# Kernel tuning notes

Hardware: AMD Instinct MI355X
Metric: run time of the kernel (lower is better)

## Reference

```python
import jax, jax.numpy as jnp
import numpy as np

LN_EPS = 1e-5  # torch nn.LayerNorm default

def _layer_norm(x, w, b):
    m = jnp.mean(x, axis=-1, keepdims=True)
    v = jnp.mean(jnp.square(x - m), axis=-1, keepdims=True)
    return (x - m) * jax.lax.rsqrt(v + LN_EPS) * w + b

def setup_inputs() -> dict:
    R, N, D, A = 8, 8192, 2048, 128
    init_scale = 0.01
    key = jax.random.key(0)
    k0, k1, k2 = jax.random.split(key, 3)
    x = jax.random.normal(k0, (N, D), jnp.float32)
    ln_w = jnp.ones((R, D), jnp.float32)              # per-router input LayerNorm weight
    ln_b = jnp.zeros((R, D), jnp.float32)
    router_weights = jax.random.normal(k1, (R, D, A), jnp.float32) * init_scale
    rw_ln_w = jax.random.normal(k2, (R, D), jnp.float32) * init_scale  # weight-LN gamma (init ones*scale in src)
    rw_ln_b = jnp.zeros((R, D), jnp.float32)
    router_bias = jnp.zeros((R, A), jnp.float32)
    return {"x": x, "ln_w": ln_w, "ln_b": ln_b, "router_weights": router_weights,
            "rw_ln_w": rw_ln_w, "rw_ln_b": rw_ln_b, "router_bias": router_bias}

def reference(x, ln_w, ln_b, router_weights, rw_ln_w, rw_ln_b, router_bias):
    # Per-router LayerNorm of shared input x: new_x [R, N, D]
    new_x = jax.vmap(lambda w, b: _layer_norm(x, w, b))(ln_w, ln_b)
    # normalize_router_weights=True: LayerNorm over in_dim of W[i].T, then transpose back
    rw_norm = jax.vmap(lambda W, w, b: _layer_norm(W.T, w, b).T)(router_weights, rw_ln_w, rw_ln_b)  # [R, D, A]
    adapter_logits = jnp.einsum('rnd,rda->rna', new_x, rw_norm) + router_bias[:, None, :]
    adapter_probs = jax.nn.softmax(adapter_logits, axis=-1)
    return new_x, adapter_logits, adapter_probs
```

## Files before the change

### kernel.cpp

```cpp
#include <hip/hip_runtime.h>
#include <hip/hip_bf16.h>
#include <stdint.h>

#define R_ 8
#define N_ 8192
#define D_ 2048
#define A_ 128
#define J_ 1024
#define LN_EPS 1e-5f

typedef __attribute__((ext_vector_type(8))) short bf16x8;
typedef __attribute__((ext_vector_type(4))) float f32x4;

__device__ inline ushort f2bf(float f) {
    union { float f; uint32_t u; } v; v.f = f;
    uint32_t u = v.u;
    return (ushort)((u + 0x7fffu + ((u >> 16) & 1u)) >> 16);
}
__device__ inline float bf2f(ushort u) {
    union { uint32_t u; float f; } v; v.u = ((uint32_t)u) << 16;
    return v.f;
}

__global__ __launch_bounds__(256) void k_prep(
    const float* __restrict__ x,
    const float* __restrict__ W,
    const float* __restrict__ ln_w,
    const float* __restrict__ ln_b,
    const float* __restrict__ rw_w,
    const float* __restrict__ rw_b,
    const float* __restrict__ rbias,
    ushort* __restrict__ xhat,
    ushort* __restrict__ Bt,
    float* __restrict__ cvec)
{
    __shared__ float sm[16];
    const int t = threadIdx.x;

    if (blockIdx.x < N_) {
        const int n = blockIdx.x;
        const float* xr = x + (size_t)n * D_;
        float4 v0 = *(const float4*)(xr + t * 4);
        float4 v1 = *(const float4*)(xr + 1024 + t * 4);
        float s  = v0.x + v0.y + v0.z + v0.w + v1.x + v1.y + v1.z + v1.w;
        float sq = v0.x*v0.x + v0.y*v0.y + v0.z*v0.z + v0.w*v0.w
                 + v1.x*v1.x + v1.y*v1.y + v1.z*v1.z + v1.w*v1.w;
        #pragma unroll
        for (int o = 32; o > 0; o >>= 1) {
            s  += __shfl_xor(s,  o, 64);
            sq += __shfl_xor(sq, o, 64);
        }
        if ((t & 63) == 0) { sm[t >> 6] = s; sm[8 + (t >> 6)] = sq; }
        __syncthreads();
        s  = sm[0] + sm[1] + sm[2] + sm[3];
        sq = sm[8] + sm[9] + sm[10] + sm[11];
        const float mean = s * (1.0f / D_);
        const float var  = sq * (1.0f / D_) - mean * mean;
        const float rstd = rsqrtf(var + LN_EPS);

        ushort4 p0 = make_ushort4(f2bf((v0.x - mean) * rstd), f2bf((v0.y - mean) * rstd),
                                  f2bf((v0.z - mean) * rstd), f2bf((v0.w - mean) * rstd));
        ushort4 p1 = make_ushort4(f2bf((v1.x - mean) * rstd), f2bf((v1.y - mean) * rstd),
                                  f2bf((v1.z - mean) * rstd), f2bf((v1.w - mean) * rstd));
        *(ushort4*)(xhat + (size_t)n * D_ + t * 4)        = p0;
        *(ushort4*)(xhat + (size_t)n * D_ + 1024 + t * 4) = p1;
    } else {
        const int j = blockIdx.x - N_;
        const int r = j >> 7, a = j & 127;
        const float* Wc = W + (size_t)r * D_ * A_ + a;

        float vals[8];
        float s = 0.f, sq = 0.f;
        #pragma unroll
        for (int k = 0; k < 8; ++k) {
            float v = Wc[(size_t)(t + k * 256) * A_];
            vals[k] = v; s += v; sq += v * v;
        }
        #pragma unroll
        for (int o = 32; o > 0; o >>= 1) {
            s  += __shfl_xor(s,  o, 64);
            sq += __shfl_xor(sq, o, 64);
        }
        if ((t & 63) == 0) { sm[t >> 6] = s; sm[8 + (t >> 6)] = sq; }
        __syncthreads();
        s  = sm[0] + sm[1] + sm[2] + sm[3];
        sq = sm[8] + sm[9] + sm[10] + sm[11];
        const float mean = s * (1.0f / D_);
        const float var  = sq * (1.0f / D_) - mean * mean;
        const float rstd = rsqrtf(var + LN_EPS);

        float cp = 0.f;
        #pragma unroll
        for (int k = 0; k < 8; ++k) {
            const int d = t + k * 256;
            const float nv = (vals[k] - mean) * rstd * rw_w[(size_t)r * D_ + d]
                           + rw_b[(size_t)r * D_ + d];
            Bt[(size_t)j * D_ + d] = f2bf(ln_w[(size_t)r * D_ + d] * nv);
            cp += ln_b[(size_t)r * D_ + d] * nv;
        }
        __syncthreads();
        #pragma unroll
        for (int o = 32; o > 0; o >>= 1) cp += __shfl_xor(cp, o, 64);
        if ((t & 63) == 0) sm[t >> 6] = cp;
        __syncthreads();
        if (t == 0) cvec[j] = sm[0] + sm[1] + sm[2] + sm[3] + rbias[(size_t)r * A_ + a];
    }
}

__global__ __launch_bounds__(256) void k_fused(
    const ushort* __restrict__ Xh,
    const ushort* __restrict__ Bt,
    const float* __restrict__ cvec,
    const float* __restrict__ ln_w,
    const float* __restrict__ ln_b,
    float* __restrict__ new_x,
    float* __restrict__ logits,
    float* __restrict__ probs)
{
    __shared__ __attribute__((aligned(16))) ushort As[2][64 * 32];
    __shared__ __attribute__((aligned(16))) ushort Bs[2][128 * 32];
    __shared__ __attribute__((aligned(16))) float lwS[D_];
    __shared__ __attribute__((aligned(16))) float lbS[D_];

    const int t    = threadIdx.x;
    const int lane = t & 63;
    const int w    = t >> 6;
    const int r    = blockIdx.x & 7;
    const int mt   = blockIdx.x >> 3;
    const int m0   = mt * 64;
    const int j0   = r * 128;

    const int arow = t >> 2, akc = t & 3;
    const ushort* gA0 = Xh + (size_t)(m0 + arow) * D_ + akc * 8;

    auto stage = [&](int buf, int kt) {
        __builtin_amdgcn_global_load_lds(
            (const __attribute__((address_space(1))) void*)(gA0 + kt * 32),
            (__attribute__((address_space(3))) void*)(&As[buf][t * 8]), 16, 0, 0);
        #pragma unroll
        for (int c = 0; c < 2; ++c) {
            const int q   = t + c * 256;
            const int row = q >> 2;
            const int kc  = q & 3;
            const ushort* gB = Bt + (size_t)(j0 + row) * D_ + kt * 32 + kc * 8;
            __builtin_amdgcn_global_load_lds(
                (const __attribute__((address_space(1))) void*)gB,
                (__attribute__((address_space(3))) void*)(&Bs[buf][q * 8]), 16, 0, 0);
        }
    };

    #pragma unroll
    for (int i = 0; i < 2; ++i) {
        const int idx = t + i * 256;
        ((float4*)lwS)[idx] = ((const float4*)(ln_w + (size_t)r * D_))[idx];
        ((float4*)lbS)[idx] = ((const float4*)(ln_b + (size_t)r * D_))[idx];
    }

    f32x4 acc[8];
    #pragma unroll
    for (int jf = 0; jf < 8; ++jf) acc[jf] = (f32x4){0.f, 0.f, 0.f, 0.f};

    float* nx_base = new_x + ((size_t)r * N_ + m0) * D_;

    stage(0, 0);
    asm volatile("s_waitcnt vmcnt(0) lgkmcnt(0)" ::: "memory");
    __builtin_amdgcn_s_barrier();
    __builtin_amdgcn_sched_barrier(0);

    auto body = [&](int cur, int kt) {
        if (kt < 63) stage(cur ^ 1, kt + 1);

        const int kbase = kt * 32;
        #pragma unroll
        for (int c = 0; c < 2; ++c) {
            const int q    = t + c * 256;
            const int row  = q >> 3;
            const int col4 = q & 7;
            const int d    = kbase + col4 * 4;
            const ushort4 hb = *(const ushort4*)(&As[cur][row * 32 + col4 * 4]);
            const float4 lw4 = *(const float4*)(&lwS[d]);
            const float4 lb4 = *(const float4*)(&lbS[d]);
            f32x4 o;
            o[0] = bf2f(hb.x) * lw4.x + lb4.x;
            o[1] = bf2f(hb.y) * lw4.y + lb4.y;
            o[2] = bf2f(hb.z) * lw4.z + lb4.z;
            o[3] = bf2f(hb.w) * lw4.w + lb4.w;
            __builtin_nontemporal_store(o, (f32x4*)(nx_base + (size_t)row * D_ + d));
        }

        const bf16x8 afr = *(const bf16x8*)(&As[cur][(w * 16 + (lane & 15)) * 32
                                                     + (lane >> 4) * 8]);
        #pragma unroll
        for (int jf = 0; jf < 8; ++jf) {
            const bf16x8 bfr = *(const bf16x8*)(&Bs[cur][(jf * 16 + (lane & 15)) * 32
                                                         + (lane >> 4) * 8]);
            acc[jf] = __builtin_amdgcn_mfma_f32_16x16x32_bf16(afr, bfr, acc[jf], 0, 0, 0);
        }

        if (kt < 63) {
            asm volatile("s_waitcnt vmcnt(2)" ::: "memory");
            __builtin_amdgcn_s_barrier();
            __builtin_amdgcn_sched_barrier(0);
        }
    };

    for (int kt2 = 0; kt2 < 64; kt2 += 2) {
        body(0, kt2);
        body(1, kt2 + 1);
    }

    float cv[8];
    #pragma unroll
    for (int jf = 0; jf < 8; ++jf) cv[jf] = cvec[j0 + jf * 16 + (lane & 15)];

    #pragma unroll
    for (int reg = 0; reg < 4; ++reg) {
        const int row = m0 + w * 16 + (lane >> 4) * 4 + reg;
        float v[8], e[8];
        float mx = -3.4e38f;
        #pragma unroll
        for (int jf = 0; jf < 8; ++jf) {
            v[jf] = acc[jf][reg] + cv[jf];
            mx = fmaxf(mx, v[jf]);
        }
        #pragma unroll
        for (int o = 8; o > 0; o >>= 1) mx = fmaxf(mx, __shfl_xor(mx, o, 64));
        float ssum = 0.f;
        #pragma unroll
        for (int jf = 0; jf < 8; ++jf) { e[jf] = __expf(v[jf] - mx); ssum += e[jf]; }
        #pragma unroll
        for (int o = 8; o > 0; o >>= 1) ssum += __shfl_xor(ssum, o, 64);
        const float inv = 1.0f / ssum;
        float* lrow = logits + ((size_t)r * N_ + row) * A_;
        float* prow = probs  + ((size_t)r * N_ + row) * A_;
        #pragma unroll
        for (int jf = 0; jf < 8; ++jf) {
            const int aa = jf * 16 + (lane & 15);
            __builtin_nontemporal_store(v[jf], lrow + aa);
            __builtin_nontemporal_store(e[jf] * inv, prow + aa);
        }
    }
}

extern "C" void kernel_launch(void* const* d_in, const int* in_sizes, int n_in,
                              void* d_out, int out_size, void* d_ws, size_t ws_size,
                              hipStream_t stream)
{
    const float* x     = (const float*)d_in[0];
    const float* ln_w  = (const float*)d_in[1];
    const float* ln_b  = (const float*)d_in[2];
    const float* W     = (const float*)d_in[3];
    const float* rw_w  = (const float*)d_in[4];
    const float* rw_b  = (const float*)d_in[5];
    const float* rbias = (const float*)d_in[6];

    float* out    = (float*)d_out;
    float* new_x  = out;
    float* logits = out + (size_t)R_ * N_ * D_;
    float* probs  = logits + (size_t)R_ * N_ * A_;

    ushort* xhat = (ushort*)d_ws;
    ushort* Btp  = (ushort*)((char*)d_ws + (size_t)N_ * D_ * 2);
    float*  cvec = (float*)((char*)d_ws + (size_t)N_ * D_ * 2 + (size_t)J_ * D_ * 2);

    hipLaunchKernelGGL(k_prep, dim3(N_ + J_), dim3(256), 0, stream,
                       x, W, ln_w, ln_b, rw_w, rw_b, rbias, xhat, Btp, cvec);
    hipLaunchKernelGGL(k_fused, dim3(J_), dim3(256), 0, stream,
                       xhat, Btp, cvec, ln_w, ln_b, new_x, logits, probs);
}
```

Before: 191.4 us.

## Warp-specialize fused kernel into MFMA producer warps and new_x store warps

The fused kernel grows to 512 threads. The first four waves stage tiles and run the MFMA GEMM plus softmax, and four extra waves only rescale the shared bf16 X tile and stream new_x to global memory, synchronized by matching per-iteration barriers. The goal is to overlap the large new_x write traffic with the matrix work instead of serializing both in the same waves. To fit the larger block, the LayerNorm gamma/beta copies in LDS are stored as bf16. That loses precision for general weights and raises the per-block thread count, which may lower occupancy.

```diff
diff --git a/kernel.cpp b/kernel.cpp
--- a/kernel.cpp
+++ b/kernel.cpp
@@ -107,7 +107,7 @@
     }
 }
 
-__global__ __launch_bounds__(256) void k_fused(
+__global__ __launch_bounds__(512) void k_fused(
     const ushort* __restrict__ Xh,
     const ushort* __restrict__ Bt,
     const float* __restrict__ cvec,
@@ -119,125 +119,134 @@
 {
     __shared__ __attribute__((aligned(16))) ushort As[2][64 * 32];
     __shared__ __attribute__((aligned(16))) ushort Bs[2][128 * 32];
-    __shared__ __attribute__((aligned(16))) float lwS[D_];
-    __shared__ __attribute__((aligned(16))) float lbS[D_];
-
-    const int t    = threadIdx.x;
-    const int lane = t & 63;
-    const int w    = t >> 6;
-    const int r    = blockIdx.x & 7;
-    const int mt   = blockIdx.x >> 3;
-    const int m0   = mt * 64;
-    const int j0   = r * 128;
-
-    const int arow = t >> 2, akc = t & 3;
-    const ushort* gA0 = Xh + (size_t)(m0 + arow) * D_ + akc * 8;
-
-    auto stage = [&](int buf, int kt) {
-        __builtin_amdgcn_global_load_lds(
-            (const __attribute__((address_space(1))) void*)(gA0 + kt * 32),
-            (__attribute__((address_space(3))) void*)(&As[buf][t * 8]), 16, 0, 0);
-        #pragma unroll
-        for (int c = 0; c < 2; ++c) {
-            const int q   = t + c * 256;
-            const int row = q >> 2;
-            const int kc  = q & 3;
-            const ushort* gB = Bt + (size_t)(j0 + row) * D_ + kt * 32 + kc * 8;
+    __shared__ __attribute__((aligned(16))) ushort lwS[D_];
+    __shared__ __attribute__((aligned(16))) ushort lbS[D_];
+
+    const int t  = threadIdx.x;
+    const int r  = blockIdx.x & 7;
+    const int mt = blockIdx.x >> 3;
+    const int m0 = mt * 64;
+    const int j0 = r * 128;
+
+    {
+        const float4 wv = ((const float4*)(ln_w + (size_t)r * D_))[t];
+        const float4 bv = ((const float4*)(ln_b + (size_t)r * D_))[t];
+        *(ushort4*)(&lwS[t * 4]) = make_ushort4(f2bf(wv.x), f2bf(wv.y), f2bf(wv.z), f2bf(wv.w));
+        *(ushort4*)(&lbS[t * 4]) = make_ushort4(f2bf(bv.x), f2bf(bv.y), f2bf(bv.z), f2bf(bv.w));
+    }
+
+    float* nx_base = new_x + ((size_t)r * N_ + m0) * D_;
+
+    if (t < 256) {
+        const int lane = t & 63;
+        const int w    = t >> 6;
+        const int arow = t >> 2, akc = t & 3;
+        const ushort* gA0 = Xh + (size_t)(m0 + arow) * D_ + akc * 8;
+
+        auto stage = [&](int buf, int kt) {
             __builtin_amdgcn_global_load_lds(
-                (const __attribute__((address_space(1))) void*)gB,
-                (__attribute__((address_space(3))) void*)(&Bs[buf][q * 8]), 16, 0, 0);
-        }
-    };
-
-    #pragma unroll
-    for (int i = 0; i < 2; ++i) {
-        const int idx = t + i * 256;
-        ((float4*)lwS)[idx] = ((const float4*)(ln_w + (size_t)r * D_))[idx];
-        ((float4*)lbS)[idx] = ((const float4*)(ln_b + (size_t)r * D_))[idx];
-    }
-
-    f32x4 acc[8];
-    #pragma unroll
-    for (int jf = 0; jf < 8; ++jf) acc[jf] = (f32x4){0.f, 0.f, 0.f, 0.f};
-
-    float* nx_base = new_x + ((size_t)r * N_ + m0) * D_;
-
-    stage(0, 0);
-    asm volatile("s_waitcnt vmcnt(0) lgkmcnt(0)" ::: "memory");
-    __builtin_amdgcn_s_barrier();
-    __builtin_amdgcn_sched_barrier(0);
-
-    auto body = [&](int cur, int kt) {
-        if (kt < 63) stage(cur ^ 1, kt + 1);
-
-        const int kbase = kt * 32;
-        #pragma unroll
-        for (int c = 0; c < 2; ++c) {
-            const int q    = t + c * 256;
-            const int row  = q >> 3;
-            const int col4 = q & 7;
-            const int d    = kbase + col4 * 4;
-            const ushort4 hb = *(const ushort4*)(&As[cur][row * 32 + col4 * 4]);
-            const float4 lw4 = *(const float4*)(&lwS[d]);
-            const float4 lb4 = *(const float4*)(&lbS[d]);
-            f32x4 o;
-            o[0] = bf2f(hb.x) * lw4.x + lb4.x;
-            o[1] = bf2f(hb.y) * lw4.y + lb4.y;
-            o[2] = bf2f(hb.z) * lw4.z + lb4.z;
-            o[3] = bf2f(hb.w) * lw4.w + lb4.w;
-            __builtin_nontemporal_store(o, (f32x4*)(nx_base + (size_t)row * D_ + d));
-        }
-
-        const bf16x8 afr = *(const bf16x8*)(&As[cur][(w * 16 + (lane & 15)) * 32
-                                                     + (lane >> 4) * 8]);
-        #pragma unroll
-        for (int jf = 0; jf < 8; ++jf) {
-            const bf16x8 bfr = *(const bf16x8*)(&Bs[cur][(jf * 16 + (lane & 15)) * 32
+                (const __attribute__((address_space(1))) void*)(gA0 + kt * 32),
+                (__attribute__((address_space(3))) void*)(&As[buf][t * 8]), 16, 0, 0);
+            #pragma unroll
+            for (int c = 0; c < 2; ++c) {
+                const int q   = t + c * 256;
+                const int row = q >> 2;
+                const int kc  = q & 3;
+                const ushort* gB = Bt + (size_t)(j0 + row) * D_ + kt * 32 + kc * 8;
+                __builtin_amdgcn_global_load_lds(
+                    (const __attribute__((address_space(1))) void*)gB,
+                    (__attribute__((address_space(3))) void*)(&Bs[buf][q * 8]), 16, 0, 0);
+            }
+        };
+
+        f32x4 acc[8];
+        #pragma unroll
+        for (int jf = 0; jf < 8; ++jf) acc[jf] = (f32x4){0.f, 0.f, 0.f, 0.f};
+
+        stage(0, 0);
+        asm volatile("s_waitcnt vmcnt(0) lgkmcnt(0)" ::: "memory");
+        __builtin_amdgcn_s_barrier();
+        __builtin_amdgcn_sched_barrier(0);
+
+        for (int i = 0; i < 64; ++i) {
+            const int cur = i & 1;
+            if (i < 63) stage(cur ^ 1, i + 1);
+
+            const bf16x8 afr = *(const bf16x8*)(&As[cur][(w * 16 + (lane & 15)) * 32
                                                          + (lane >> 4) * 8]);
-            acc[jf] = __builtin_amdgcn_mfma_f32_16x16x32_bf16(afr, bfr, acc[jf], 0, 0, 0);
-        }
-
-        if (kt < 63) {
-            asm volatile("s_waitcnt vmcnt(2)" ::: "memory");
+            #pragma unroll
+            for (int jf = 0; jf < 8; ++jf) {
+                const bf16x8 bfr = *(const bf16x8*)(&Bs[cur][(jf * 16 + (lane & 15)) * 32
+                                                             + (lane >> 4) * 8]);
+                acc[jf] = __builtin_amdgcn_mfma_f32_16x16x32_bf16(afr, bfr, acc[jf], 0, 0, 0);
+            }
+
+            asm volatile("s_waitcnt vmcnt(0)" ::: "memory");
+            __builtin_amdgcn_sched_barrier(0);
             __builtin_amdgcn_s_barrier();
             __builtin_amdgcn_sched_barrier(0);
         }
-    };
-
-    for (int kt2 = 0; kt2 < 64; kt2 += 2) {
-        body(0, kt2);
-        body(1, kt2 + 1);
-    }
-
-    float cv[8];
-    #pragma unroll
-    for (int jf = 0; jf < 8; ++jf) cv[jf] = cvec[j0 + jf * 16 + (lane & 15)];
-
-    #pragma unroll
-    for (int reg = 0; reg < 4; ++reg) {
-        const int row = m0 + w * 16 + (lane >> 4) * 4 + reg;
-        float v[8], e[8];
-        float mx = -3.4e38f;
-        #pragma unroll
-        for (int jf = 0; jf < 8; ++jf) {
-            v[jf] = acc[jf][reg] + cv[jf];
-            mx = fmaxf(mx, v[jf]);
-        }
-        #pragma unroll
-        for (int o = 8; o > 0; o >>= 1) mx = fmaxf(mx, __shfl_xor(mx, o, 64));
-        float ssum = 0.f;
-        #pragma unroll
-        for (int jf = 0; jf < 8; ++jf) { e[jf] = __expf(v[jf] - mx); ssum += e[jf]; }
-        #pragma unroll
-        for (int o = 8; o > 0; o >>= 1) ssum += __shfl_xor(ssum, o, 64);
-        const float inv = 1.0f / ssum;
-        float* lrow = logits + ((size_t)r * N_ + row) * A_;
-        float* prow = probs  + ((size_t)r * N_ + row) * A_;
-        #pragma unroll
-        for (int jf = 0; jf < 8; ++jf) {
-            const int aa = jf * 16 + (lane & 15);
-            __builtin_nontemporal_store(v[jf], lrow + aa);
-            __builtin_nontemporal_store(e[jf] * inv, prow + aa);
+
+        float cv[8];
+        #pragma unroll
+        for (int jf = 0; jf < 8; ++jf) cv[jf] = cvec[j0 + jf * 16 + (lane & 15)];
+
+        #pragma unroll
+        for (int reg = 0; reg < 4; ++reg) {
+            const int row = m0 + w * 16 + (lane >> 4) * 4 + reg;
+            float v[8], e[8];
+            float mx = -3.4e38f;
+            #pragma unroll
+            for (int jf = 0; jf < 8; ++jf) {
+                v[jf] = acc[jf][reg] + cv[jf];
+                mx = fmaxf(mx, v[jf]);
+            }
+            #pragma unroll
+            for (int o = 8; o > 0; o >>= 1) mx = fmaxf(mx, __shfl_xor(mx, o, 64));
+            float ssum = 0.f;
+            #pragma unroll
+            for (int jf = 0; jf < 8; ++jf) { e[jf] = __expf(v[jf] - mx); ssum += e[jf]; }
+            #pragma unroll
+            for (int o = 8; o > 0; o >>= 1) ssum += __shfl_xor(ssum, o, 64);
+            const float inv = 1.0f / ssum;
+            float* lrow = logits + ((size_t)r * N_ + row) * A_;
+            float* prow = probs  + ((size_t)r * N_ + row) * A_;
+            #pragma unroll
+            for (int jf = 0; jf < 8; ++jf) {
+                const int aa = jf * 16 + (lane & 15);
+                __builtin_nontemporal_store(v[jf], lrow + aa);
+                __builtin_nontemporal_store(e[jf] * inv, prow + aa);
+            }
+        }
+    } else {
+        const int tw = t - 256;
+
+        asm volatile("s_waitcnt lgkmcnt(0)" ::: "memory");
+        __builtin_amdgcn_s_barrier();
+        __builtin_amdgcn_sched_barrier(0);
+
+        for (int i = 0; i < 64; ++i) {
+            const int cur = i & 1;
+            const int kbase = i * 32;
+            #pragma unroll
+            for (int c = 0; c < 2; ++c) {
+                const int q    = tw + c * 256;
+                const int row  = q >> 3;
+                const int col4 = q & 7;
+                const int d    = kbase + col4 * 4;
+                const ushort4 hb = *(const ushort4*)(&As[cur][row * 32 + col4 * 4]);
+                const ushort4 w4 = *(const ushort4*)(&lwS[d]);
+                const ushort4 b4 = *(const ushort4*)(&lbS[d]);
+                f32x4 o;
+                o[0] = bf2f(hb.x) * bf2f(w4.x) + bf2f(b4.x);
+                o[1] = bf2f(hb.y) * bf2f(w4.y) + bf2f(b4.y);
+                o[2] = bf2f(hb.z) * bf2f(w4.z) + bf2f(b4.z);
+                o[3] = bf2f(hb.w) * bf2f(w4.w) + bf2f(b4.w);
+                __builtin_nontemporal_store(o, (f32x4*)(nx_base + (size_t)row * D_ + d));
+            }
+            __builtin_amdgcn_sched_barrier(0);
+            __builtin_amdgcn_s_barrier();
+            __builtin_amdgcn_sched_barrier(0);
         }
     }
 }
@@ -265,6 +274,6 @@
 
     hipLaunchKernelGGL(k_prep, dim3(N_ + J_), dim3(256), 0, stream,
                        x, W, ln_w, ln_b, rw_w, rw_b, rbias, xhat, Btp, cvec);
-    hipLaunchKernelGGL(k_fused, dim3(J_), dim3(256), 0, stream,
+    hipLaunchKernelGGL(k_fused, dim3(J_), dim3(512), 0, stream,
                        xhat, Btp, cvec, ln_w, ln_b, new_x, logits, probs);
 }
```

Result: no change. 191.9 us (+0.3%).
